# Performance work log

Measured on AMD Instinct MI355X. Metric: run time of the kernel, lower is better.

## Reference

```python
import jax, jax.numpy as jnp
import numpy as np
from jax import lax

L, B, S, D, H = 2, 8, 2048, 1024, 1024
LOG_H0 = float(np.log(0.5))  # h0 = g(0) = 0.5


def _log_g(x):
    # log of g(x) = x + 0.5 if x >= 0 else sigmoid(x)
    return jnp.where(x >= 0, jnp.log(jnp.where(x >= 0, x + 0.5, 1.0)), -jax.nn.softplus(-x))


def _mingru_layer(x, Wz, bz, Wh, bh):
    # x: (B,S,D) -> (B,S,H) via log-space heinsen associative scan
    k = jnp.einsum('bsd,hd->bsh', x, Wz) + bz          # gate pre-activation
    log_z = -jax.nn.softplus(-k)                        # log sigmoid(k)
    log_coeffs = -jax.nn.softplus(k)                    # log (1 - sigmoid(k))
    pre_h = jnp.einsum('bsd,hd->bsh', x, Wh) + bh
    log_values = log_z + _log_g(pre_h)                  # log(z * h_tilde)
    Bq = x.shape[0]
    # prepend initial state: coeff 0 (log 1), value log(h0)
    log_coeffs = jnp.pad(log_coeffs, ((0, 0), (1, 0), (0, 0)))
    log_values = jnp.concatenate(
        [jnp.full((Bq, 1, log_values.shape[-1]), LOG_H0, dtype=log_values.dtype), log_values], axis=1)
    a_star = jnp.cumsum(log_coeffs, axis=1)
    log_h = a_star + lax.cumlogsumexp(log_values - a_star, axis=1)
    return jnp.exp(log_h)[:, 1:]


def setup_inputs() -> dict:
    key = jax.random.key(0)
    ks = jax.random.split(key, 5)
    stdv = 1.0 / np.sqrt(D)
    u = lambda k, shp: jax.random.uniform(k, shp, jnp.float32, -stdv, stdv)
    return {
        'x': jax.random.normal(ks[0], (B, S, D), jnp.float32),
        'Wz': u(ks[1], (L, H, D)),
        'bz': u(ks[2], (L, H)),
        'Wh': u(ks[3], (L, H, D)),
        'bh': u(ks[4], (L, H)),
    }


def reference(x, Wz, bz, Wh, bh):
    h = x
    for l in range(Wz.shape[0]):
        h = _mingru_layer(h, Wz[l], bz[l], Wh[l], bh[l])
    return h  # (B,S,H), last layer outputs
```

## Files before the change

### kernel.cpp

```cpp
#include <hip/hip_runtime.h>
#include <hip/hip_bf16.h>
#include <hip/hip_cooperative_groups.h>


#define L_ 2
#define B_ 8
#define S_ 2048
#define D_ 1024
#define H_ 1024
#define M_ (B_*S_)
#define NC 32
#define CL (S_/NC)

typedef __bf16    bf16x8 __attribute__((ext_vector_type(8)));
typedef float     f32x4  __attribute__((ext_vector_type(4)));
typedef _Float16  h2     __attribute__((ext_vector_type(2)));
typedef _Float16  h8     __attribute__((ext_vector_type(8)));

__device__ __forceinline__ ushort f2bf(float f) {
    union { __hip_bfloat16 h; ushort u; } c;
    c.h = __float2bfloat16(f);
    return c.u;
}

__device__ __forceinline__ void async16(const void* g, void* l) {
    __builtin_amdgcn_global_load_lds(
        (const __attribute__((address_space(1))) unsigned int*)g,
        (__attribute__((address_space(3))) unsigned int*)l, 16, 0, 0);
}

__global__ __launch_bounds__(256) void cast_all(const float* __restrict__ x,
                                                const float* __restrict__ Wz,
                                                const float* __restrict__ Wh,
                                                ushort* __restrict__ xb,
                                                ushort* __restrict__ wzb,
                                                ushort* __restrict__ whb) {
    const int nw = L_*H_*D_/4;
    int i = blockIdx.x * 256 + threadIdx.x;
    {
        float4 v = ((const float4*)x)[i];
        ushort4 o;
        o.x = f2bf(v.x); o.y = f2bf(v.y); o.z = f2bf(v.z); o.w = f2bf(v.w);
        ((ushort4*)xb)[i] = o;
    }
    if (i < nw) {
        float4 v = ((const float4*)Wz)[i];
        ushort4 o;
        o.x = f2bf(v.x); o.y = f2bf(v.y); o.z = f2bf(v.z); o.w = f2bf(v.w);
        ((ushort4*)wzb)[i] = o;
        float4 w = ((const float4*)Wh)[i];
        ushort4 p;
        p.x = f2bf(w.x); p.y = f2bf(w.y); p.z = f2bf(w.z); p.w = f2bf(w.w);
        ((ushort4*)whb)[i] = p;
    }
}

#define SWZ(R, c) (((R) << 6) + ((((c) ^ ((R) & 7))) << 3))
#define MFMA16 __builtin_amdgcn_mfma_f32_16x16x32_bf16

__global__ __launch_bounds__(256, 2) void mingru_layer(const ushort* A,
                                                       const ushort* __restrict__ Wz,
                                                       const ushort* __restrict__ Wh,
                                                       const float* __restrict__ bz,
                                                       const float* __restrict__ bh,
                                                       float* Ac,
                                                       float* Bc,
                                                       float* outf,
                                                       ushort* outb,
                                                       int write_bf16)
{
    extern __shared__ __align__(16) ushort sm[];

    const int t    = threadIdx.x;
    const int lane = t & 63;
    const int wave = t >> 6;
    const int bid  = (int)blockIdx.x;
    const int xcd  = bid & 7;
    const int q8   = bid >> 3;
    const int nblk = q8 & 15;
    const int pg   = q8 >> 4;
    const int panel = pg*8 + xcd;
    const int b    = panel >> 2;
    const int mg   = panel & 3;
    const int n0 = nblk * 64;
    const int wm = (wave >> 1) * 64;
    const int wn = (wave & 1) * 32;

    const int srow   = lane >> 3;
    const int scol_g = (((lane & 7) ^ srow) << 3);
    const int lrow = lane & 15;
    const int lcq  = lane >> 4;
    const int colq = lane & 15;
    const int rowq = (lane >> 4) << 2;

    float bzv[2], bhv[2];
    #pragma unroll
    for (int nt = 0; nt < 2; ++nt) {
        const int n = n0 + wn + nt*16 + colq;
        bzv[nt] = bz[n];
        bhv[nt] = bh[n];
    }

    h8 cvr[4][8];

    #pragma unroll
    for (int ti = 0; ti < 4; ++ti) {
        const int tloc = mg*4 + ti;
        const int m0 = b*S_ + tloc*128;

        f32x4 accz[4][2] = {};
        f32x4 acch[4][2] = {};

        for (int kb = 0; kb < D_; kb += 64) {
            __syncthreads();
            #pragma unroll
            for (int i_ = 0; i_ < 4; ++i_) {
                int r_ = i_*32 + wave*8;
                async16(&A[(size_t)(m0 + r_ + srow)*D_ + kb + scol_g], &sm[r_*64]);
            }
            #pragma unroll
            for (int i_ = 0; i_ < 2; ++i_) {
                int r_ = i_*32 + wave*8;
                async16(&Wz[(size_t)(n0 + r_ + srow)*D_ + kb + scol_g], &sm[8192  + r_*64]);
                async16(&Wh[(size_t)(n0 + r_ + srow)*D_ + kb + scol_g], &sm[12288 + r_*64]);
            }
            __syncthreads();
            #pragma unroll
            for (int kk = 0; kk < 64; kk += 32) {
                const int cq = (kk >> 3) + lcq;
                bf16x8 af[4];
                #pragma unroll
                for (int mt = 0; mt < 4; ++mt) {
                    int R = wm + mt*16 + lrow;
                    uint4 u = *(const uint4*)&sm[SWZ(R, cq)];
                    af[mt] = __builtin_bit_cast(bf16x8, u);
                }
                #pragma unroll
                for (int nt = 0; nt < 2; ++nt) {
                    int R = wn + nt*16 + lrow;
                    uint4 uz = *(const uint4*)&sm[8192  + SWZ(R, cq)];
                    uint4 uh = *(const uint4*)&sm[12288 + SWZ(R, cq)];
                    bf16x8 zb = __builtin_bit_cast(bf16x8, uz);
                    bf16x8 hb = __builtin_bit_cast(bf16x8, uh);
                    #pragma unroll
                    for (int mt = 0; mt < 4; ++mt) {
                        accz[mt][nt] = MFMA16(af[mt], zb, accz[mt][nt], 0, 0, 0);
                        acch[mt][nt] = MFMA16(af[mt], hb, acch[mt][nt], 0, 0, 0);
                    }
                }
            }
        }

        __syncthreads();
        float2* seg = (float2*)sm;
        #pragma unroll
        for (int nt = 0; nt < 2; ++nt) {
            #pragma unroll
            for (int mt = 0; mt < 4; ++mt) {
                float a = 1.f, bb = 0.f;
                h8 pk;
                #pragma unroll
                for (int r = 0; r < 4; ++r) {
                    float kx = accz[mt][nt][r] + bzv[nt];
                    float p  = acch[mt][nt][r] + bhv[nt];
                    float e   = __expf(-fabsf(kx));
                    float inv = 1.0f / (1.0f + e);
                    float z   = (kx >= 0.f) ? inv     : e * inv;
                    float c   = (kx >= 0.f) ? e * inv : inv;
                    float g;
                    if (p >= 0.f) g = p + 0.5f;
                    else { float eg = __expf(p); g = eg / (1.0f + eg); }
                    float v = z * g;
                    pk[2*r]     = (_Float16)c;
                    pk[2*r + 1] = (_Float16)v;
                    bb = fmaf(c, bb, v);
                    a *= c;
                }
                cvr[ti][nt*4 + mt] = pk;
                const int sidx = (wm >> 2) + mt*4 + (rowq >> 2);
                seg[sidx*65 + wn + nt*16 + colq] = make_float2(a, bb);
            }
        }
        __syncthreads();
        if (t < 128) {
            const int col  = t & 63;
            const int half = t >> 6;
            float a = 1.f, bb = 0.f;
            #pragma unroll
            for (int s = 0; s < 16; ++s) {
                float2 e2 = seg[(half*16 + s)*65 + col];
                bb = fmaf(e2.x, bb, e2.y);
                a *= e2.x;
            }
            const int chunk = tloc*2 + half;
            const int qi = (b*NC + chunk)*H_ + n0 + col;
            __hip_atomic_store(&Ac[qi], a,  __ATOMIC_RELAXED, __HIP_MEMORY_SCOPE_AGENT);
            __hip_atomic_store(&Bc[qi], bb, __ATOMIC_RELAXED, __HIP_MEMORY_SCOPE_AGENT);
        }
    }

    __threadfence();
    cooperative_groups::this_grid().sync();

    h2* cvlds = (h2*)sm;
    #pragma unroll
    for (int ti = 0; ti < 4; ++ti) {
        const int tloc = mg*4 + ti;
        const int m0 = b*S_ + tloc*128;
        __syncthreads();
        #pragma unroll
        for (int nt = 0; nt < 2; ++nt) {
            const int coll = wn + nt*16 + colq;
            #pragma unroll
            for (int mt = 0; mt < 4; ++mt) {
                h8 pk = cvr[ti][nt*4 + mt];
                #pragma unroll
                for (int r = 0; r < 4; ++r) {
                    const int rr = wm + mt*16 + rowq + r;
                    h2 e; e[0] = pk[2*r]; e[1] = pk[2*r + 1];
                    cvlds[rr*64 + coll] = e;
                }
            }
        }
        __syncthreads();
        if (t < 128) {
            const int col = t & 63;
            const int ck  = t >> 6;
            const int cg  = tloc*2 + ck;
            float hc = 0.5f;
            for (int cp = 0; cp < cg; ++cp) {
                int idx = (b*NC + cp)*H_ + n0 + col;
                float av = __hip_atomic_load(&Ac[idx], __ATOMIC_RELAXED, __HIP_MEMORY_SCOPE_AGENT);
                float bv = __hip_atomic_load(&Bc[idx], __ATOMIC_RELAXED, __HIP_MEMORY_SCOPE_AGENT);
                hc = fmaf(av, hc, bv);
            }
            const size_t gbase = (size_t)(m0 + ck*64)*H_ + n0 + col;
            if (write_bf16) {
                #pragma unroll 4
                for (int row = 0; row < 64; ++row) {
                    h2 e = cvlds[(ck*64 + row)*64 + col];
                    hc = fmaf((float)e[0], hc, (float)e[1]);
                    outb[gbase + (size_t)row*H_] = f2bf(hc);
                }
            } else {
                #pragma unroll 4
                for (int row = 0; row < 64; ++row) {
                    h2 e = cvlds[(ck*64 + row)*64 + col];
                    hc = fmaf((float)e[0], hc, (float)e[1]);
                    outf[gbase + (size_t)row*H_] = hc;
                }
            }
        }
    }
}

__global__ __launch_bounds__(256) void gemm_fb(const ushort* __restrict__ A,
                                               const ushort* __restrict__ Wz,
                                               const ushort* __restrict__ Wh,
                                               const float* __restrict__ bz,
                                               const float* __restrict__ bh,
                                               h2* __restrict__ cv,
                                               float* __restrict__ Ac,
                                               float* __restrict__ Bc)
{
    __shared__ __align__(16) ushort sm[16384];

    const int t    = threadIdx.x;
    const int lane = t & 63;
    const int wave = t >> 6;
    const int xcd = (int)blockIdx.x & 7;
    const int k8  = (int)blockIdx.x >> 3;
    const int nblk = k8 & 15;
    const int mblk = ((k8 >> 4) << 3) + xcd;
    const int m0 = mblk * 128;
    const int n0 = nblk * 64;
    const int wm = (wave >> 1) * 64;
    const int wn = (wave & 1) * 32;

    const int srow   = lane >> 3;
    const int scol_g = (((lane & 7) ^ srow) << 3);

    f32x4 accz[4][2] = {};
    f32x4 acch[4][2] = {};
    const int lrow = lane & 15;
    const int lcq  = lane >> 4;

    for (int kb = 0; kb < D_; kb += 64) {
        __syncthreads();
        #pragma unroll
        for (int i = 0; i < 4; ++i) {
            int r = i*32 + wave*8;
            async16(&A[(size_t)(m0 + r + srow)*D_ + kb + scol_g], &sm[r*64]);
        }
        #pragma unroll
        for (int i = 0; i < 2; ++i) {
            int r = i*32 + wave*8;
            async16(&Wz[(size_t)(n0 + r + srow)*D_ + kb + scol_g], &sm[8192  + r*64]);
            async16(&Wh[(size_t)(n0 + r + srow)*D_ + kb + scol_g], &sm[12288 + r*64]);
        }
        __syncthreads();
        #pragma unroll
        for (int kk = 0; kk < 64; kk += 32) {
            const int cq = (kk >> 3) + lcq;
            bf16x8 af[4];
            #pragma unroll
            for (int mt = 0; mt < 4; ++mt) {
                int R = wm + mt*16 + lrow;
                uint4 u = *(const uint4*)&sm[SWZ(R, cq)];
                af[mt] = __builtin_bit_cast(bf16x8, u);
            }
            #pragma unroll
            for (int nt = 0; nt < 2; ++nt) {
                int R = wn + nt*16 + lrow;
                uint4 uz = *(const uint4*)&sm[8192  + SWZ(R, cq)];
                uint4 uh = *(const uint4*)&sm[12288 + SWZ(R, cq)];
                bf16x8 zb = __builtin_bit_cast(bf16x8, uz);
                bf16x8 hb = __builtin_bit_cast(bf16x8, uh);
                #pragma unroll
                for (int mt = 0; mt < 4; ++mt) {
                    accz[mt][nt] = MFMA16(af[mt], zb, accz[mt][nt], 0, 0, 0);
                    acch[mt][nt] = MFMA16(af[mt], hb, acch[mt][nt], 0, 0, 0);
                }
            }
        }
    }

    __syncthreads();
    float2* seg = (float2*)sm;
    const int colq = lane & 15;
    const int rowq = (lane >> 4) << 2;
    #pragma unroll
    for (int nt = 0; nt < 2; ++nt) {
        const int n = n0 + wn + nt*16 + colq;
        const float bzv = bz[n];
        const float bhv = bh[n];
        #pragma unroll
        for (int mt = 0; mt < 4; ++mt) {
            float a = 1.f, bb = 0.f;
            h8 pk;
            #pragma unroll
            for (int r = 0; r < 4; ++r) {
                float kx = accz[mt][nt][r] + bzv;
                float p  = acch[mt][nt][r] + bhv;
                float e   = __expf(-fabsf(kx));
                float inv = 1.0f / (1.0f + e);
                float z   = (kx >= 0.f) ? inv     : e * inv;
                float c   = (kx >= 0.f) ? e * inv : inv;
                float g;
                if (p >= 0.f) g = p + 0.5f;
                else { float eg = __expf(p); g = eg / (1.0f + eg); }
                float v = z * g;
                pk[2*r]     = (_Float16)c;
                pk[2*r + 1] = (_Float16)v;
                bb = fmaf(c, bb, v);
                a *= c;
            }
            const int mb4 = (m0 + wm + mt*16 + rowq) >> 2;
            *(h8*)&cv[((size_t)mb4 * H_ + n) * 4] = pk;
            const int sidx = (wm >> 2) + mt*4 + (rowq >> 2);
            seg[sidx*65 + wn + nt*16 + colq] = make_float2(a, bb);
        }
    }
    __syncthreads();
    if (t < 128) {
        const int col  = t & 63;
        const int half = t >> 6;
        float a = 1.f, bb = 0.f;
        #pragma unroll
        for (int s = 0; s < 16; ++s) {
            float2 e2 = seg[(half*16 + s)*65 + col];
            bb = fmaf(e2.x, bb, e2.y);
            a *= e2.x;
        }
        const int b     = m0 >> 11;
        const int chunk = ((m0 >> 6) & (NC - 1)) + half;
        const int q = (b*NC + chunk)*H_ + n0 + col;
        Ac[q] = a; Bc[q] = bb;
    }
}

__global__ __launch_bounds__(256) void scan_emit_fb(const h2* __restrict__ cv,
                                                    const float* __restrict__ Ac,
                                                    const float* __restrict__ Bc,
                                                    float* __restrict__ outf,
                                                    ushort* __restrict__ outb,
                                                    const int write_bf16)
{
    int q = blockIdx.x * 256 + threadIdx.x;
    int h = q & (H_-1);
    int c = (q >> 10) & (NC-1);
    int b = q >> 15;
    float hc = 0.5f;
    for (int cp = 0; cp < c; ++cp) {
        int idx = (b*NC + cp)*H_ + h;
        hc = fmaf(Ac[idx], hc, Bc[idx]);
    }
    const int mb = b*S_ + c*CL;
    if (write_bf16) {
        #pragma unroll 4
        for (int j = 0; j < 16; ++j) {
            h8 e = *(const h8*)&cv[(((size_t)(mb >> 2) + j)*H_ + h) * 4];
            #pragma unroll
            for (int u = 0; u < 4; ++u) {
                hc = fmaf((float)e[2*u], hc, (float)e[2*u + 1]);
                outb[(size_t)(mb + 4*j + u)*H_ + h] = f2bf(hc);
            }
        }
    } else {
        #pragma unroll 4
        for (int j = 0; j < 16; ++j) {
            h8 e = *(const h8*)&cv[(((size_t)(mb >> 2) + j)*H_ + h) * 4];
            #pragma unroll
            for (int u = 0; u < 4; ++u) {
                hc = fmaf((float)e[2*u], hc, (float)e[2*u + 1]);
                outf[(size_t)(mb + 4*j + u)*H_ + h] = hc;
            }
        }
    }
}

extern "C" void kernel_launch(void* const* d_in, const int* in_sizes, int n_in,
                              void* d_out, int out_size, void* d_ws, size_t ws_size,
                              hipStream_t stream)
{
    const float* x  = (const float*)d_in[0];
    const float* Wz = (const float*)d_in[1];
    const float* bz = (const float*)d_in[2];
    const float* Wh = (const float*)d_in[3];
    const float* bh = (const float*)d_in[4];
    float* out = (float*)d_out;

    ushort* xb  = (ushort*)d_ws;
    ushort* wzb = xb  + (size_t)M_*D_;
    ushort* whb = wzb + (size_t)L_*H_*D_;
    h2*     cv  = (h2*)(whb + (size_t)L_*H_*D_);
    float*  Ac  = (float*)(cv + (size_t)M_*H_);
    float*  Bc  = Ac + B_*NC*H_;

    static int coop_ok = -1;
    if (coop_ok < 0) {
        int nb = 0;
        hipError_t e = hipOccupancyMaxActiveBlocksPerMultiprocessor(
            &nb, reinterpret_cast<const void*>(mingru_layer), 256, (size_t)32768);
        coop_ok = (e == hipSuccess && nb >= 2) ? 1 : 0;
    }

    cast_all<<<(M_*D_/4)/256, 256, 0, stream>>>(x, Wz, Wh, xb, wzb, whb);

    if (coop_ok) {
        for (int l = 0; l < L_; ++l) {
            const ushort* A_  = xb;
            const ushort* Wz_ = wzb + (size_t)l*H_*D_;
            const ushort* Wh_ = whb + (size_t)l*H_*D_;
            const float*  bz_ = bz + l*H_;
            const float*  bh_ = bh + l*H_;
            float*  Ac_ = Ac;
            float*  Bc_ = Bc;
            float*  of_ = out;
            ushort* ob_ = xb;
            int wb = (l == 0) ? 1 : 0;
            void* args[] = {&A_, &Wz_, &Wh_, &bz_, &bh_, &Ac_, &Bc_, &of_, &ob_, &wb};
            hipLaunchCooperativeKernel(reinterpret_cast<const void*>(mingru_layer),
                                       dim3(512), dim3(256), args, 32768, stream);
        }
    } else {
        const int gemm_grid = (M_/128) * (H_/64);
        for (int l = 0; l < L_; ++l) {
            gemm_fb<<<gemm_grid, 256, 0, stream>>>(xb,
                                                   wzb + (size_t)l*H_*D_,
                                                   whb + (size_t)l*H_*D_,
                                                   bz + l*H_, bh + l*H_,
                                                   cv, Ac, Bc);
            scan_emit_fb<<<(B_*NC*H_)/256, 256, 0, stream>>>(cv, Ac, Bc, out, xb,
                                                             (l == 0) ? 1 : 0);
        }
    }
}
```

Before: 337.5 us.

## Spill gate coefficients to global memory and parallelize emit phase across all threads

Instead of holding per-tile (coeff, value) pairs in registers across the grid barrier and rescanning via LDS with half the threads, the GEMM phase writes packed fp16 pairs to a global buffer. After the grid sync, every thread handles one (batch, chunk, channel) sequence, reading the pairs from global memory and emitting outputs. This frees the large register cache and uses the full grid for the scan. In exchange it adds a global round-trip of the intermediate buffer per layer. It also replaces atomic loads and stores with plain accesses and moves to static shared memory.

```diff
diff --git a/kernel.cpp b/kernel.cpp
--- a/kernel.cpp
+++ b/kernel.cpp
@@ -63,50 +63,35 @@
                                                        const ushort* __restrict__ Wh,
                                                        const float* __restrict__ bz,
                                                        const float* __restrict__ bh,
+                                                       h2* __restrict__ cv,
                                                        float* Ac,
                                                        float* Bc,
                                                        float* outf,
                                                        ushort* outb,
                                                        int write_bf16)
 {
-    extern __shared__ __align__(16) ushort sm[];
+    __shared__ __align__(16) ushort sm[16384];
 
     const int t    = threadIdx.x;
     const int lane = t & 63;
     const int wave = t >> 6;
-    const int bid  = (int)blockIdx.x;
-    const int xcd  = bid & 7;
-    const int q8   = bid >> 3;
-    const int nblk = q8 & 15;
-    const int pg   = q8 >> 4;
-    const int panel = pg*8 + xcd;
-    const int b    = panel >> 2;
-    const int mg   = panel & 3;
-    const int n0 = nblk * 64;
+    const int lrow = lane & 15;
+    const int lcq  = lane >> 4;
+    const int srow   = lane >> 3;
+    const int scol_g = (((lane & 7) ^ srow) << 3);
+    const int colq = lane & 15;
+    const int rowq = (lane >> 4) << 2;
     const int wm = (wave >> 1) * 64;
     const int wn = (wave & 1) * 32;
 
-    const int srow   = lane >> 3;
-    const int scol_g = (((lane & 7) ^ srow) << 3);
-    const int lrow = lane & 15;
-    const int lcq  = lane >> 4;
-    const int colq = lane & 15;
-    const int rowq = (lane >> 4) << 2;
-
-    float bzv[2], bhv[2];
-    #pragma unroll
-    for (int nt = 0; nt < 2; ++nt) {
-        const int n = n0 + wn + nt*16 + colq;
-        bzv[nt] = bz[n];
-        bhv[nt] = bh[n];
-    }
-
-    h8 cvr[4][8];
-
-    #pragma unroll
-    for (int ti = 0; ti < 4; ++ti) {
-        const int tloc = mg*4 + ti;
-        const int m0 = b*S_ + tloc*128;
+    for (int rep = 0; rep < 4; ++rep) {
+        const int bid2 = (int)blockIdx.x + (rep << 9);
+        const int xcd = bid2 & 7;
+        const int k8  = bid2 >> 3;
+        const int nblk = k8 & 15;
+        const int mblk = ((k8 >> 4) << 3) + xcd;
+        const int m0 = mblk * 128;
+        const int n0 = nblk * 64;
 
         f32x4 accz[4][2] = {};
         f32x4 acch[4][2] = {};
@@ -114,15 +99,15 @@
         for (int kb = 0; kb < D_; kb += 64) {
             __syncthreads();
             #pragma unroll
-            for (int i_ = 0; i_ < 4; ++i_) {
-                int r_ = i_*32 + wave*8;
-                async16(&A[(size_t)(m0 + r_ + srow)*D_ + kb + scol_g], &sm[r_*64]);
-            }
-            #pragma unroll
-            for (int i_ = 0; i_ < 2; ++i_) {
-                int r_ = i_*32 + wave*8;
-                async16(&Wz[(size_t)(n0 + r_ + srow)*D_ + kb + scol_g], &sm[8192  + r_*64]);
-                async16(&Wh[(size_t)(n0 + r_ + srow)*D_ + kb + scol_g], &sm[12288 + r_*64]);
+            for (int i = 0; i < 4; ++i) {
+                int r = i*32 + wave*8;
+                async16(&A[(size_t)(m0 + r + srow)*D_ + kb + scol_g], &sm[r*64]);
+            }
+            #pragma unroll
+            for (int i = 0; i < 2; ++i) {
+                int r = i*32 + wave*8;
+                async16(&Wz[(size_t)(n0 + r + srow)*D_ + kb + scol_g], &sm[8192  + r*64]);
+                async16(&Wh[(size_t)(n0 + r + srow)*D_ + kb + scol_g], &sm[12288 + r*64]);
             }
             __syncthreads();
             #pragma unroll
@@ -155,14 +140,17 @@
         float2* seg = (float2*)sm;
         #pragma unroll
         for (int nt = 0; nt < 2; ++nt) {
+            const int n = n0 + wn + nt*16 + colq;
+            const float bzv = bz[n];
+            const float bhv = bh[n];
             #pragma unroll
             for (int mt = 0; mt < 4; ++mt) {
                 float a = 1.f, bb = 0.f;
                 h8 pk;
                 #pragma unroll
                 for (int r = 0; r < 4; ++r) {
-                    float kx = accz[mt][nt][r] + bzv[nt];
-                    float p  = acch[mt][nt][r] + bhv[nt];
+                    float kx = accz[mt][nt][r] + bzv;
+                    float p  = acch[mt][nt][r] + bhv;
                     float e   = __expf(-fabsf(kx));
                     float inv = 1.0f / (1.0f + e);
                     float z   = (kx >= 0.f) ? inv     : e * inv;
@@ -176,7 +164,8 @@
                     bb = fmaf(c, bb, v);
                     a *= c;
                 }
-                cvr[ti][nt*4 + mt] = pk;
+                const int mb4 = (m0 + wm + mt*16 + rowq) >> 2;
+                *(h8*)&cv[((size_t)mb4 * H_ + n) * 4] = pk;
                 const int sidx = (wm >> 2) + mt*4 + (rowq >> 2);
                 seg[sidx*65 + wn + nt*16 + colq] = make_float2(a, bb);
             }
@@ -192,62 +181,46 @@
                 bb = fmaf(e2.x, bb, e2.y);
                 a *= e2.x;
             }
-            const int chunk = tloc*2 + half;
+            const int b     = m0 >> 11;
+            const int chunk = ((m0 >> 6) & (NC - 1)) + half;
             const int qi = (b*NC + chunk)*H_ + n0 + col;
-            __hip_atomic_store(&Ac[qi], a,  __ATOMIC_RELAXED, __HIP_MEMORY_SCOPE_AGENT);
-            __hip_atomic_store(&Bc[qi], bb, __ATOMIC_RELAXED, __HIP_MEMORY_SCOPE_AGENT);
+            Ac[qi] = a; Bc[qi] = bb;
         }
     }
 
     __threadfence();
     cooperative_groups::this_grid().sync();
 
-    h2* cvlds = (h2*)sm;
     #pragma unroll
-    for (int ti = 0; ti < 4; ++ti) {
-        const int tloc = mg*4 + ti;
-        const int m0 = b*S_ + tloc*128;
-        __syncthreads();
-        #pragma unroll
-        for (int nt = 0; nt < 2; ++nt) {
-            const int coll = wn + nt*16 + colq;
-            #pragma unroll
-            for (int mt = 0; mt < 4; ++mt) {
-                h8 pk = cvr[ti][nt*4 + mt];
-                #pragma unroll
-                for (int r = 0; r < 4; ++r) {
-                    const int rr = wm + mt*16 + rowq + r;
-                    h2 e; e[0] = pk[2*r]; e[1] = pk[2*r + 1];
-                    cvlds[rr*64 + coll] = e;
-                }
-            }
-        }
-        __syncthreads();
-        if (t < 128) {
-            const int col = t & 63;
-            const int ck  = t >> 6;
-            const int cg  = tloc*2 + ck;
-            float hc = 0.5f;
-            for (int cp = 0; cp < cg; ++cp) {
-                int idx = (b*NC + cp)*H_ + n0 + col;
-                float av = __hip_atomic_load(&Ac[idx], __ATOMIC_RELAXED, __HIP_MEMORY_SCOPE_AGENT);
-                float bv = __hip_atomic_load(&Bc[idx], __ATOMIC_RELAXED, __HIP_MEMORY_SCOPE_AGENT);
-                hc = fmaf(av, hc, bv);
-            }
-            const size_t gbase = (size_t)(m0 + ck*64)*H_ + n0 + col;
-            if (write_bf16) {
-                #pragma unroll 4
-                for (int row = 0; row < 64; ++row) {
-                    h2 e = cvlds[(ck*64 + row)*64 + col];
-                    hc = fmaf((float)e[0], hc, (float)e[1]);
-                    outb[gbase + (size_t)row*H_] = f2bf(hc);
-                }
-            } else {
-                #pragma unroll 4
-                for (int row = 0; row < 64; ++row) {
-                    h2 e = cvlds[(ck*64 + row)*64 + col];
-                    hc = fmaf((float)e[0], hc, (float)e[1]);
-                    outf[gbase + (size_t)row*H_] = hc;
+    for (int rep = 0; rep < 2; ++rep) {
+        const int q = (int)blockIdx.x * 256 + t + rep * 131072;
+        const int h = q & (H_-1);
+        const int c = (q >> 10) & (NC-1);
+        const int b = q >> 15;
+        float hc = 0.5f;
+        for (int cp = 0; cp < c; ++cp) {
+            int idx = (b*NC + cp)*H_ + h;
+            hc = fmaf(Ac[idx], hc, Bc[idx]);
+        }
+        const int mb = b*S_ + c*CL;
+        if (write_bf16) {
+            #pragma unroll 4
+            for (int j = 0; j < 16; ++j) {
+                h8 e = *(const h8*)&cv[(((size_t)(mb >> 2) + j)*H_ + h) * 4];
+                #pragma unroll
+                for (int u = 0; u < 4; ++u) {
+                    hc = fmaf((float)e[2*u], hc, (float)e[2*u + 1]);
+                    outb[(size_t)(mb + 4*j + u)*H_ + h] = f2bf(hc);
+                }
+            }
+        } else {
+            #pragma unroll 4
+            for (int j = 0; j < 16; ++j) {
+                h8 e = *(const h8*)&cv[(((size_t)(mb >> 2) + j)*H_ + h) * 4];
+                #pragma unroll
+                for (int u = 0; u < 4; ++u) {
+                    hc = fmaf((float)e[2*u], hc, (float)e[2*u + 1]);
+                    outf[(size_t)(mb + 4*j + u)*H_ + h] = hc;
                 }
             }
         }
@@ -441,7 +414,7 @@
     if (coop_ok < 0) {
         int nb = 0;
         hipError_t e = hipOccupancyMaxActiveBlocksPerMultiprocessor(
-            &nb, reinterpret_cast<const void*>(mingru_layer), 256, (size_t)32768);
+            &nb, reinterpret_cast<const void*>(mingru_layer), 256, (size_t)0);
         coop_ok = (e == hipSuccess && nb >= 2) ? 1 : 0;
     }
 
@@ -454,14 +427,16 @@
             const ushort* Wh_ = whb + (size_t)l*H_*D_;
             const float*  bz_ = bz + l*H_;
             const float*  bh_ = bh + l*H_;
+            h2*     cv_ = cv;
             float*  Ac_ = Ac;
             float*  Bc_ = Bc;
             float*  of_ = out;
             ushort* ob_ = xb;
             int wb = (l == 0) ? 1 : 0;
-            void* args[] = {&A_, &Wz_, &Wh_, &bz_, &bh_, &Ac_, &Bc_, &of_, &ob_, &wb};
+            void* args[] = {&A_, &Wz_, &Wh_, &bz_, &bh_, &cv_, &Ac_, &Bc_,
+                            &of_, &ob_, &wb};
             hipLaunchCooperativeKernel(reinterpret_cast<const void*>(mingru_layer),
-                                       dim3(512), dim3(256), args, 32768, stream);
+                                       dim3(512), dim3(256), args, 0, stream);
         }
     } else {
         const int gemm_grid = (M_/128) * (H_/64);
```

After: 333.6 us. Within noise of the previous version (-1.2%).
